# Kernel optimization log

Measured on AMD Instinct MI355X. Metric: run time of the kernel, lower is better.

## Reference

```python
import jax, jax.numpy as jnp
import numpy as np

N_AUDIO = 32768  # n_audio_samples


def upsample_linear(x, out_size):
    """torch F.interpolate(mode='linear', align_corners=False) along last axis."""
    t = x.shape[-1]
    pos = (jnp.arange(out_size, dtype=x.dtype) + 0.5) * (t / out_size) - 0.5
    pos = jnp.clip(pos, 0.0, t - 1)
    i0 = jnp.floor(pos).astype(jnp.int32)
    i1 = jnp.minimum(i0 + 1, t - 1)
    w = pos - i0.astype(x.dtype)
    return jnp.take(x, i0, axis=-1) * (1.0 - w) + jnp.take(x, i1, axis=-1) * w


def setup_inputs() -> dict:
    key = jax.random.key(0)
    k1, k2, k3, k4, k5 = jax.random.split(key, 5)
    B, C, T, N_OSC = 8, 128, 128, 128
    x = jax.random.normal(k1, (B, C, T), dtype=jnp.float32)
    # conv1d kernel_size=1 weights -> plain [out, in] matrices + bias
    amp_w = jax.random.normal(k2, (N_OSC, C), dtype=jnp.float32) * 0.08
    amp_b = jax.random.normal(k3, (N_OSC,), dtype=jnp.float32) * 0.08
    freq_w = jax.random.normal(k4, (N_OSC, C), dtype=jnp.float32) * 0.08
    freq_b = jax.random.normal(k5, (N_OSC,), dtype=jnp.float32) * 0.08
    return {"x": x, "amp_w": amp_w, "amp_b": amp_b, "freq_w": freq_w, "freq_b": freq_b}


def reference(x, amp_w, amp_b, freq_w, freq_b):
    # 1x1 conv == per-frame matmul: [B,C,T] x [O,C] -> [B,O,T]
    amp = jax.nn.sigmoid(jnp.einsum('bct,oc->bot', x, amp_w) + amp_b[None, :, None])
    freq = jax.nn.sigmoid(jnp.einsum('bct,oc->bot', x, freq_w) + freq_b[None, :, None])
    # upsample control signals to audio rate: [B,O,T] -> [B,O,N_AUDIO]
    amp = upsample_linear(amp, N_AUDIO)
    freq = upsample_linear(freq, N_AUDIO)
    # additive synthesis: cumulative phase -> sin -> amp -> mean over oscillators
    phase = jnp.cumsum(freq * jnp.pi, axis=-1)
    audio = jnp.sin(phase) * amp
    return jnp.mean(audio, axis=1, keepdims=True)  # [B,1,N_AUDIO]
```

## Files before the change

### kernel.cpp

```cpp
#include <hip/hip_runtime.h>
#include <hip/hip_bf16.h>
#include <math.h>

#define N_AUDIO 32768
#define NB 8
#define NC 128
#define NT 128
#define NO 128


__global__ __launch_bounds__(128)
void prep_kernel(const float* __restrict__ x,
                 const float* __restrict__ amp_w,
                 const float* __restrict__ amp_b,
                 const float* __restrict__ freq_w,
                 const float* __restrict__ freq_b,
                 float4* __restrict__ SEG,
                 float*  __restrict__ CW)
{
    const int bo = blockIdx.x;
    const int b  = bo >> 7;
    const int o  = bo & 127;
    const int t  = threadIdx.x;

    const float* xp = x + b * (NC * NT) + t;
    const float* wa = amp_w  + o * NC;
    const float* wf = freq_w + o * NC;

    float va = 0.f, vf = 0.f;
#pragma unroll 8
    for (int c = 0; c < NC; ++c) {
        float xv = xp[c * NT];
        va = fmaf(xv, wa[c], va);
        vf = fmaf(xv, wf[c], vf);
    }
    va += amp_b[o];
    vf += freq_b[o];
    const float sa = 1.f / (1.f + __expf(-va));
    const float sf = 1.f / (1.f + __expf(-vf));

    __shared__ float  fsh[NT];
    __shared__ float  ash[NT];
    __shared__ double psh[NT];
    fsh[t] = sf;
    ash[t] = sa;
    psh[t] = (double)sf;
    __syncthreads();

    for (int off = 1; off < NT; off <<= 1) {
        double add = (t >= off) ? psh[t - off] : 0.0;
        double v   = psh[t];
        __syncthreads();
        psh[t] = v + add;
        __syncthreads();
    }
    const double incl = psh[t];
    const double excl = incl - (double)sf;
    double Cd = 256.0 * excl + 128.0 * (double)sf;
    Cd = fmod(Cd, 2.0);

    const float df = (t < NT - 1) ? (fsh[t + 1] - sf) : 0.f;
    const float da = (t < NT - 1) ? (ash[t + 1] - sa) : 0.f;

    const int idx = (b * NT + t) * NO + o;
    SEG[idx] = make_float4(sf, df, sa, da);
    CW[idx]  = (float)Cd;
}

__global__ __launch_bounds__(256)
void synth_kernel(const float4* __restrict__ SEG,
                  const float*  __restrict__ CW,
                  float* __restrict__ out)
{
    const int j = blockIdx.x * 256 + threadIdx.x;
    const int b = blockIdx.y;

    int   i;
    float m, mask;
    if (j < 128)          { i = 0;   m = (float)(j - 127);   mask = 0.f; }
    else if (j >= 32640)  { i = 127; m = (float)(j - 32639); mask = 0.f; }
    else {
        const int jj = j - 128;
        i    = jj >> 8;
        m    = (float)((jj & 255) + 1);
        mask = 1.f;
    }

    const float m2s = m * m * (1.f / 512.f) * mask;
    const float wA  = (m - 0.5f) * (1.f / 256.f) * mask;

    const float4* seg  = SEG + (b * NT + i) * NO;
    const float*  crow = CW  + (b * NT + i) * NO;

    float sum = 0.f;
#pragma unroll 4
    for (int o = 0; o < NO; ++o) {
        const float4 s  = seg[o];
        const float  Cv = crow[o];
        const float  z   = fmaf(s.y, m2s, fmaf(m, s.x, Cv));
        const float  amp = fmaf(s.w, wA, s.z);
        float tt = z * 0.5f;
        tt -= floorf(tt);
        sum = fmaf(amp, __builtin_amdgcn_sinf(tt), sum);
    }
    out[b * N_AUDIO + j] = sum * (1.f / 128.f);
}

extern "C" void kernel_launch(void* const* d_in, const int* in_sizes, int n_in,
                              void* d_out, int out_size, void* d_ws, size_t ws_size,
                              hipStream_t stream)
{
    const float* x      = (const float*)d_in[0];
    const float* amp_w  = (const float*)d_in[1];
    const float* amp_b  = (const float*)d_in[2];
    const float* freq_w = (const float*)d_in[3];
    const float* freq_b = (const float*)d_in[4];
    float* out = (float*)d_out;

    float4* SEG = (float4*)d_ws;
    float*  CW  = (float*)((char*)d_ws + (size_t)NB * NT * NO * sizeof(float4));

    prep_kernel<<<dim3(NB * NO), dim3(128), 0, stream>>>(
        x, amp_w, amp_b, freq_w, freq_b, SEG, CW);
    synth_kernel<<<dim3(N_AUDIO / 256, NB), dim3(256), 0, stream>>>(SEG, CW, out);
}
```

Before: 91.54 us.

## Prescale segment coefficients and stage per-block segment rows in LDS

Folds the constant scales (half-phase, 1/512 curvature, 1/128 mean) into the per-segment coefficients in the prep kernel, so the synth inner loop loses a multiply and the fract reduces to a single fract instruction. The phase offset is now reduced with floor instead of fmod. The synth kernel loads the two segment rows a block needs into shared memory once, rather than each thread reading global memory, and splits the oscillator sum into two accumulators for more ILP. This relies on each 256-sample block touching only two segments, and the boundary-handling indexing was reworked to fit that layout.

After: 80.41 us. 1.14x faster.

```diff
diff --git a/kernel.cpp b/kernel.cpp
--- a/kernel.cpp
+++ b/kernel.cpp
@@ -56,14 +56,17 @@
     }
     const double incl = psh[t];
     const double excl = incl - (double)sf;
-    double Cd = 256.0 * excl + 128.0 * (double)sf;
-    Cd = fmod(Cd, 2.0);
+    double Cd = 128.0 * excl + 64.0 * (double)sf;
+    Cd -= floor(Cd);
 
     const float df = (t < NT - 1) ? (fsh[t + 1] - sf) : 0.f;
     const float da = (t < NT - 1) ? (ash[t + 1] - sa) : 0.f;
 
     const int idx = (b * NT + t) * NO + o;
-    SEG[idx] = make_float4(sf, df, sa, da);
+    SEG[idx] = make_float4(0.5f * sf,
+                           df * (1.f / 1024.f),
+                           sa * (1.f / 128.f),
+                           da * (1.f / 128.f));
     CW[idx]  = (float)Cd;
 }
 
@@ -72,38 +75,48 @@
                   const float*  __restrict__ CW,
                   float* __restrict__ out)
 {
-    const int j = blockIdx.x * 256 + threadIdx.x;
-    const int b = blockIdx.y;
+    const int k   = blockIdx.x;
+    const int b   = blockIdx.y;
+    const int tid = threadIdx.x;
+    const int j   = k * 256 + tid;
 
-    int   i;
+    __shared__ float4 sP[2][NO];
+    __shared__ float  sC[2][NO];
+    {
+        const int h   = tid >> 7;
+        const int oo  = tid & 127;
+        const int row = h ? k : (k > 0 ? k - 1 : 0);
+        const int base = (b * NT + row) * NO;
+        sP[h][oo] = SEG[base + oo];
+        sC[h][oo] = CW[base + oo];
+    }
+    __syncthreads();
+
     float m, mask;
-    if (j < 128)          { i = 0;   m = (float)(j - 127);   mask = 0.f; }
-    else if (j >= 32640)  { i = 127; m = (float)(j - 32639); mask = 0.f; }
-    else {
-        const int jj = j - 128;
-        i    = jj >> 8;
-        m    = (float)((jj & 255) + 1);
-        mask = 1.f;
+    if (j < 128) { m = (float)(j - 127); mask = 0.f; }
+    else         { m = (float)(((j - 128) & 255) + 1); mask = 1.f; }
+    const float m2 = m * m * mask;
+    const float wA = (m - 0.5f) * (1.f / 256.f) * mask;
+
+    const int h = tid >> 7;
+    const float4* __restrict__ P = sP[h];
+    const float*  __restrict__ C = sC[h];
+
+    float sum0 = 0.f, sum1 = 0.f;
+#pragma unroll 4
+    for (int o = 0; o < NO; o += 2) {
+        const float4 p0 = P[o];
+        const float4 p1 = P[o + 1];
+        const float  c0 = C[o];
+        const float  c1 = C[o + 1];
+        const float z0 = fmaf(m2, p0.y, fmaf(m, p0.x, c0));
+        const float z1 = fmaf(m2, p1.y, fmaf(m, p1.x, c1));
+        const float a0 = fmaf(wA, p0.w, p0.z);
+        const float a1 = fmaf(wA, p1.w, p1.z);
+        sum0 = fmaf(a0, __builtin_amdgcn_sinf(__builtin_amdgcn_fractf(z0)), sum0);
+        sum1 = fmaf(a1, __builtin_amdgcn_sinf(__builtin_amdgcn_fractf(z1)), sum1);
     }
-
-    const float m2s = m * m * (1.f / 512.f) * mask;
-    const float wA  = (m - 0.5f) * (1.f / 256.f) * mask;
-
-    const float4* seg  = SEG + (b * NT + i) * NO;
-    const float*  crow = CW  + (b * NT + i) * NO;
-
-    float sum = 0.f;
-#pragma unroll 4
-    for (int o = 0; o < NO; ++o) {
-        const float4 s  = seg[o];
-        const float  Cv = crow[o];
-        const float  z   = fmaf(s.y, m2s, fmaf(m, s.x, Cv));
-        const float  amp = fmaf(s.w, wA, s.z);
-        float tt = z * 0.5f;
-        tt -= floorf(tt);
-        sum = fmaf(amp, __builtin_amdgcn_sinf(tt), sum);
-    }
-    out[b * N_AUDIO + j] = sum * (1.f / 128.f);
+    out[b * N_AUDIO + j] = sum0 + sum1;
 }
 
 extern "C" void kernel_launch(void* const* d_in, const int* in_sizes, int n_in,
```
